# Performance work log

Hardware: AMD Instinct MI355X
Metric: run time of the kernel (lower is better)

The kernel has to match this reference:

```python
import jax, jax.numpy as jnp
import numpy as np

EMBED_DIM = 512
NUM_HEADS = 8
HEAD_DIM = EMBED_DIM // NUM_HEADS
SEQ = 1024
BSZ = 8
T1 = 0.6
T2 = 0.4
MAX_NEG = -jnp.finfo(jnp.float32).max


def setup_inputs() -> dict:
    key = jax.random.key(0)
    ks = jax.random.split(key, 10)
    shp = (SEQ, BSZ, EMBED_DIM)
    inv = 1.0 / np.sqrt(EMBED_DIM)
    return {
        "query": jax.random.normal(ks[0], shp, jnp.float32),
        "key": jax.random.normal(ks[1], shp, jnp.float32),
        "value": jax.random.normal(ks[2], shp, jnp.float32),
        "query_sem": jax.random.normal(ks[3], shp, jnp.float32),
        "key_sem": jax.random.normal(ks[4], shp, jnp.float32),
        "sem_map": jax.random.uniform(ks[5], (SEQ, SEQ), jnp.float32),
        "in_proj_weight": jax.random.normal(ks[6], (3 * EMBED_DIM, EMBED_DIM), jnp.float32) * inv,
        "in_proj_bias": jnp.zeros((3 * EMBED_DIM,), jnp.float32),
        "out_proj_weight": jax.random.normal(ks[7], (EMBED_DIM, EMBED_DIM), jnp.float32) * inv,
        "out_proj_bias": jnp.zeros((EMBED_DIM,), jnp.float32),
    }


def _heads(x):
    # [T, B, E] -> [B*H, T, head_dim]
    T, B, E = x.shape
    return jnp.transpose(x.reshape(T, B * NUM_HEADS, HEAD_DIM), (1, 0, 2))


def _attn_path(qx, kx, vx, sem_map, Wi, bi, Wo, bo, ssa):
    # packed in-projection (generic path: q, k, v are distinct tensors)
    Wq, Wk, Wv = jnp.split(Wi, 3, axis=0)
    bq, bk, bv = jnp.split(bi, 3)
    q = _heads(qx @ Wq.T + bq)
    k = _heads(kx @ Wk.T + bk)
    v = _heads(vx @ Wv.T + bv)
    scale = 1.0 / np.sqrt(HEAD_DIM)
    scores = jnp.einsum("bte,bse->bts", q * scale, k)  # [B*H, T, S]
    scores = jnp.where(sem_map[None, :, :] < 0.5, MAX_NEG, scores)
    if ssa:
        # keep only the argmax entry per row, others set to max_neg
        idx = jnp.argmax(scores, axis=-1)  # [B*H, T]
        keep = jnp.arange(scores.shape[-1])[None, None, :] == idx[..., None]
        scores = jnp.where(keep, scores, MAX_NEG)
    w = jax.nn.softmax(scores, axis=-1)
    o = jnp.einsum("bts,bse->bte", w, v)  # [B*H, T, head_dim]
    o = jnp.transpose(o, (1, 0, 2)).reshape(SEQ, BSZ, EMBED_DIM)
    return o @ Wo.T + bo


def reference(query, key, value, query_sem, key_sem, sem_map, in_proj_weight, in_proj_bias, out_proj_weight, out_proj_bias):
    # SCA: semantic q/k attend, style value
    x_sca = _attn_path(query_sem, key_sem, value, sem_map, in_proj_weight, in_proj_bias, out_proj_weight, out_proj_bias, ssa=False)
    # SSA: content/style q/k, hard-argmax sparsified attention
    x_ssa = _attn_path(query, key, value, sem_map, in_proj_weight, in_proj_bias, out_proj_weight, out_proj_bias, ssa=True)
    return T1 * x_sca + T2 * x_ssa
```

## Files before the change

### kernel.cpp

```cpp
#include <hip/hip_runtime.h>
#include <float.h>


namespace {
constexpr int kSeq = 1024;
constexpr int kBsz = 8;
constexpr int kEmb = 512;
constexpr int kHD  = 64;
constexpr float kT1 = 0.6f;
constexpr float kT2 = 0.4f;
constexpr float kScale = 0.125f;
constexpr float kMargin = 0.125f;
constexpr int kCap = 256;
}

typedef short bf16x8 __attribute__((ext_vector_type(8)));
typedef float f32x4  __attribute__((ext_vector_type(4)));

union FragU { uint4 u4; bf16x8 f; uint u[4]; };

__device__ __forceinline__ ushort f2bf(float f) {
  uint u = __float_as_uint(f);
  u += 0x7fff + ((u >> 16) & 1);
  return (ushort)(u >> 16);
}
__device__ __forceinline__ uint pack2(float lo, float hi) {
  return (uint)f2bf(lo) | ((uint)f2bf(hi) << 16);
}
__device__ __forceinline__ float bf2f(uint h) {
  return __uint_as_float(h << 16);
}
__device__ __forceinline__ uint monokey(float v) {
  uint u = __float_as_uint(v);
  return (u & 0x80000000u) ? ~u : (u | 0x80000000u);
}

__global__ void smask_prep(const float* __restrict__ SEM,
                           unsigned long long* __restrict__ SMASK) {
  const int t = blockIdx.x;
  const int w4 = threadIdx.x >> 6;
  const int lane = threadIdx.x & 63;
#pragma unroll
  for (int i = 0; i < 4; ++i) {
    const int word = (w4 << 2) + i;
    const float v = SEM[t * kSeq + (word << 6) + lane];
    unsigned long long m = __ballot(v >= 0.5f);
    if (lane == 0) SMASK[t * 16 + word] = m;
  }
}

__global__ __launch_bounds__(256, 4) void proj_v4(
    const float* __restrict__ Xq, const float* __restrict__ Xk,
    const float* __restrict__ W, const float* __restrict__ bias,
    float* __restrict__ OutQ, float* __restrict__ OutK,
    ushort* __restrict__ ShQ, ushort* __restrict__ ShK)
{
  __shared__ float As[32 * 132];
  __shared__ float Bs[32 * 68];

  const int z = blockIdx.z;
  const float* X = z ? Xk : Xq;
  float* Out = z ? OutK : OutQ;
  ushort* shadow = z ? ShK : ShQ;
  const int woff = z << 9;
  const float sscale = z ? 1.0f : kScale;

  const int mBase = blockIdx.x << 7;
  const int nBase = blockIdx.y << 6;
  const int tid = threadIdx.x;
  const int tx = tid & 15;
  const int my = tid >> 4;
  const int ar = tid >> 1, ah = (tid & 1) << 4;
  const int br = tid >> 2, bk = (tid & 3) << 3;

  float acc[8][4];
#pragma unroll
  for (int i = 0; i < 8; ++i)
#pragma unroll
    for (int j = 0; j < 4; ++j) acc[i][j] = 0.f;

  const float* xp = X + (size_t)(mBase + ar) * kEmb + ah;
  const float* wp = W + (size_t)(woff + nBase + br) * kEmb + bk;

  float4 a0 = ((const float4*)xp)[0];
  float4 a1 = ((const float4*)xp)[1];
  float4 a2 = ((const float4*)xp)[2];
  float4 a3 = ((const float4*)xp)[3];
  float4 b0 = ((const float4*)wp)[0];
  float4 b1 = ((const float4*)wp)[1];

  for (int k0 = 0; k0 < kEmb; k0 += 32) {
    __syncthreads();
    {
      float av[16] = {a0.x, a0.y, a0.z, a0.w, a1.x, a1.y, a1.z, a1.w,
                      a2.x, a2.y, a2.z, a2.w, a3.x, a3.y, a3.z, a3.w};
#pragma unroll
      for (int i = 0; i < 16; ++i) As[(ah + i) * 132 + ar] = av[i];
      float bv[8] = {b0.x, b0.y, b0.z, b0.w, b1.x, b1.y, b1.z, b1.w};
#pragma unroll
      for (int i = 0; i < 8; ++i) Bs[(bk + i) * 68 + br] = bv[i];
    }
    __syncthreads();

    const int kn = k0 + 32;
    if (kn < kEmb) {
      a0 = ((const float4*)(xp + kn))[0];
      a1 = ((const float4*)(xp + kn))[1];
      a2 = ((const float4*)(xp + kn))[2];
      a3 = ((const float4*)(xp + kn))[3];
      b0 = ((const float4*)(wp + kn))[0];
      b1 = ((const float4*)(wp + kn))[1];
    }

#pragma unroll 8
    for (int k = 0; k < 32; ++k) {
      float4 A0 = *(const float4*)&As[k * 132 + (my << 3)];
      float4 A1 = *(const float4*)&As[k * 132 + (my << 3) + 4];
      float4 Bv = *(const float4*)&Bs[k * 68 + (tx << 2)];
      float aa[8] = {A0.x, A0.y, A0.z, A0.w, A1.x, A1.y, A1.z, A1.w};
      float bb[4] = {Bv.x, Bv.y, Bv.z, Bv.w};
#pragma unroll
      for (int i = 0; i < 8; ++i)
#pragma unroll
        for (int j = 0; j < 4; ++j)
          acc[i][j] = fmaf(aa[i], bb[j], acc[i][j]);
    }
  }

#pragma unroll
  for (int i = 0; i < 8; ++i) {
    const int m = mBase + (my << 3) + i;
#pragma unroll
    for (int j = 0; j < 4; ++j) {
      const int n = nBase + (tx << 2) + j;
      const float v = acc[i][j] + bias[woff + n];
      const int oi = (((m & 7) << 3) + (n >> 6)) * (kSeq * kHD) +
                     ((m >> 3) << 6) + (n & 63);
      Out[oi] = v;
      shadow[oi] = f2bf(v * sscale);
    }
  }
}

__global__ __launch_bounds__(256, 4) void gemm_bf16(
    const float* __restrict__ X0, const float* __restrict__ X1,
    const float* __restrict__ X2, const ushort* __restrict__ X16,
    const float* __restrict__ W, const float* __restrict__ bias,
    float* __restrict__ OutF, ushort* __restrict__ Out16,
    int woffBase, int aMode, int outMode, float scale0)
{
  __shared__ uint As[128 * 20];
  __shared__ uint Bs[64 * 20];

  const int z = blockIdx.z;
  const float* X = (z == 0) ? X0 : (z == 1) ? X1 : X2;
  const int woff = woffBase + (z << 9);
  const float scale = (z == 0) ? scale0 : 1.0f;
  const size_t zoff = (size_t)z * ((size_t)kSeq * kBsz * kEmb);

  const int mBase = blockIdx.x << 7;
  const int nBase = blockIdx.y << 6;
  const int tid = threadIdx.x;
  const int w = tid >> 6;
  const int l = tid & 63;
  const int l15 = l & 15;
  const int quad = l >> 4;
  const int wm = w & 1, wn = w >> 1;

  const int srow = tid >> 1;
  const int shalf = tid & 1;

  f32x4 acc[4][2];
#pragma unroll
  for (int mi = 0; mi < 4; ++mi)
#pragma unroll
    for (int ni = 0; ni < 2; ++ni) acc[mi][ni] = (f32x4){0.f, 0.f, 0.f, 0.f};

  uint4 qa0, qa1;
  float4 ra0, ra1, ra2, ra3;
  float4 rb0, rb1, rb2, rb3;

#define GLOAD(kk) do {                                                     \
    if (aMode == 2) {                                                      \
      const uint* src_ = (const uint*)X16 + (size_t)(mBase + srow) * 256 + \
                         ((kk) >> 1) + (shalf << 3);                       \
      qa0 = ((const uint4*)src_)[0];                                       \
      qa1 = ((const uint4*)src_)[1];                                       \
    } else {                                                               \
      const float* xp_ = X + (size_t)(mBase + srow) * kEmb + (kk) +        \
                         (shalf << 4);                                     \
      ra0 = ((const float4*)xp_)[0];                                       \
      ra1 = ((const float4*)xp_)[1];                                       \
      ra2 = ((const float4*)xp_)[2];                                       \
      ra3 = ((const float4*)xp_)[3];                                       \
    }                                                                      \
    if (tid < 128) {                                                       \
      const float* wp_ = W + (size_t)(woff + nBase + srow) * kEmb + (kk) + \
                         (shalf << 4);                                     \
      rb0 = ((const float4*)wp_)[0];                                       \
      rb1 = ((const float4*)wp_)[1];                                       \
      rb2 = ((const float4*)wp_)[2];                                       \
      rb3 = ((const float4*)wp_)[3];                                       \
    }                                                                      \
  } while (0)

  GLOAD(0);

  for (int k0 = 0; k0 < kEmb; k0 += 32) {
    uint4 ah0, ah1, bw0, bw1;
    if (aMode == 2) {
      ah0 = qa0; ah1 = qa1;
    } else {
      ah0 = make_uint4(pack2(ra0.x, ra0.y), pack2(ra0.z, ra0.w),
                       pack2(ra1.x, ra1.y), pack2(ra1.z, ra1.w));
      ah1 = make_uint4(pack2(ra2.x, ra2.y), pack2(ra2.z, ra2.w),
                       pack2(ra3.x, ra3.y), pack2(ra3.z, ra3.w));
    }
    if (tid < 128) {
      bw0 = make_uint4(pack2(rb0.x, rb0.y), pack2(rb0.z, rb0.w),
                       pack2(rb1.x, rb1.y), pack2(rb1.z, rb1.w));
      bw1 = make_uint4(pack2(rb2.x, rb2.y), pack2(rb2.z, rb2.w),
                       pack2(rb3.x, rb3.y), pack2(rb3.z, rb3.w));
    }
    __syncthreads();
    {
      uint* dst = As + srow * 20 + (shalf << 3);
      ((uint4*)dst)[0] = ah0;
      ((uint4*)dst)[1] = ah1;
      if (tid < 128) {
        uint* db = Bs + srow * 20 + (shalf << 3);
        ((uint4*)db)[0] = bw0;
        ((uint4*)db)[1] = bw1;
      }
    }
    __syncthreads();

    if (k0 + 32 < kEmb) GLOAD(k0 + 32);

    FragU aF[4], bF[2];
#pragma unroll
    for (int ni = 0; ni < 2; ++ni)
      bF[ni].u4 = *(const uint4*)(Bs + ((wn << 5) + (ni << 4) + l15) * 20 + (quad << 2));
#pragma unroll
    for (int mi = 0; mi < 4; ++mi)
      aF[mi].u4 = *(const uint4*)(As + ((wm << 6) + (mi << 4) + l15) * 20 + (quad << 2));
#pragma unroll
    for (int mi = 0; mi < 4; ++mi)
#pragma unroll
      for (int ni = 0; ni < 2; ++ni)
        acc[mi][ni] = __builtin_amdgcn_mfma_f32_16x16x32_bf16(
            aF[mi].f, bF[ni].f, acc[mi][ni], 0, 0, 0);
  }
#undef GLOAD

#pragma unroll
  for (int ni = 0; ni < 2; ++ni) {
    const int n = nBase + (wn << 5) + (ni << 4) + l15;
    const float bv = bias[woff + n];
#pragma unroll
    for (int mi = 0; mi < 4; ++mi) {
#pragma unroll
      for (int r = 0; r < 4; ++r) {
        const int m = mBase + (wm << 6) + (mi << 4) + (quad << 2) + r;
        const float v = acc[mi][ni][r] + bv;
        if (outMode == 0) {
          OutF[(size_t)m * kEmb + n] = v;
        } else {
          const int oi = (((m & 7) << 3) + (n >> 6)) * (kSeq * kHD) +
                         ((m >> 3) << 6) + (n & 63);
          Out16[zoff + oi] = f2bf(v * scale);
        }
      }
    }
  }
}

__global__ __launch_bounds__(256, 4) void sca_mfma2(
    const ushort* __restrict__ Q16, const ushort* __restrict__ K16,
    const ushort* __restrict__ V16,
    const unsigned long long* __restrict__ SMASK,
    ushort* __restrict__ MIX16)
{
  __shared__ uint ks[64 * 36];
  __shared__ uint vt[64 * 36];
  __shared__ uint ps[4][16 * 36];

  const int t0  = blockIdx.x << 6;
  const int bh  = blockIdx.y;
  const int tid = threadIdx.x;
  const int w    = tid >> 6;
  const int l    = tid & 63;
  const int l15  = l & 15;
  const int quad = l >> 4;

  const uint* Qu = (const uint*)Q16 + (size_t)bh * (kSeq * 32);
  const uint* Ku = (const uint*)K16 + (size_t)bh * (kSeq * 32);
  const uint* Vu = (const uint*)V16 + (size_t)bh * (kSeq * 32);

  FragU qf0, qf1;
  {
    const uint* qrow = Qu + (size_t)(t0 + (w << 4) + l15) * 32;
    qf0.u4 = *(const uint4*)(qrow + (quad << 2));
    qf1.u4 = *(const uint4*)(qrow + 16 + (quad << 2));
  }

  f32x4 oacc[4];
#pragma unroll
  for (int nt = 0; nt < 4; ++nt) oacc[nt] = (f32x4){0.f, 0.f, 0.f, 0.f};
  float den[4] = {0.f, 0.f, 0.f, 0.f};

  uint* psw = ps[w];

  const int sl = tid >> 2, c = tid & 3;
  const int p = tid >> 3, c7 = tid & 7;

  uint4 pk0 = ((const uint4*)(Ku + (size_t)sl * 32 + (c << 3)))[0];
  uint4 pk1 = ((const uint4*)(Ku + (size_t)sl * 32 + (c << 3)))[1];
  uint4 pv0 = *(const uint4*)(Vu + (size_t)(p << 1) * 32 + (c7 << 2));
  uint4 pv1 = *(const uint4*)(Vu + (size_t)(p << 1) * 32 + (c7 << 2) + 32);

  for (int s0 = 0, tile = 0; s0 < kSeq; s0 += 64, ++tile) {
    __syncthreads();
    {
      uint* dst = ks + sl * 36 + (c << 3);
      ((uint4*)dst)[0] = pk0;
      ((uint4*)dst)[1] = pk1;
    }
    {
      FragU A, B;
      A.u4 = pv0;
      B.u4 = pv1;
      const int Wp = (p + ((c7 & 3) << 2)) & 31;
#pragma unroll
      for (int i = 0; i < 8; ++i) {
        uint ai = (A.u[i >> 1] >> ((i & 1) << 4)) & 0xFFFF;
        uint bi = (B.u[i >> 1] >> ((i & 1) << 4)) & 0xFFFF;
        vt[((c7 << 3) + i) * 36 + Wp] = ai | (bi << 16);
      }
    }
    __syncthreads();

    if (s0 + 64 < kSeq) {
      const uint* kp = Ku + (size_t)(s0 + 64 + sl) * 32 + (c << 3);
      pk0 = ((const uint4*)kp)[0];
      pk1 = ((const uint4*)kp)[1];
      const uint* va = Vu + (size_t)(s0 + 64 + (p << 1)) * 32 + (c7 << 2);
      pv0 = *(const uint4*)va;
      pv1 = *(const uint4*)(va + 32);
    }

    unsigned long long wv[4];
#pragma unroll
    for (int r = 0; r < 4; ++r)
      wv[r] = SMASK[(size_t)(t0 + (w << 4) + (quad << 2) + r) * 16 + tile];

#pragma unroll
    for (int st = 0; st < 4; ++st) {
      f32x4 sacc = (f32x4){0.f, 0.f, 0.f, 0.f};
      const int srow = (st << 4) + l15;
      FragU kf0, kf1;
      kf0.u4 = *(const uint4*)(ks + srow * 36 + (quad << 2));
      kf1.u4 = *(const uint4*)(ks + srow * 36 + 16 + (quad << 2));
      sacc = __builtin_amdgcn_mfma_f32_16x16x32_bf16(qf0.f, kf0.f, sacc, 0, 0, 0);
      sacc = __builtin_amdgcn_mfma_f32_16x16x32_bf16(qf1.f, kf1.f, sacc, 0, 0, 0);

#pragma unroll
      for (int r = 0; r < 4; ++r) {
        const int trow = (quad << 2) + r;
        const uint bit = (uint)(wv[r] >> ((st << 4) + l15)) & 1u;
        const float val = bit ? __expf(sacc[r]) : 0.f;
        den[r] += val;
        const int W  = (st << 3) + (l15 >> 1);
        const int Wp = (W + (((trow >> 3) & 1) << 3)) & 31;
        ushort* p16 = (ushort*)(psw + trow * 36 + Wp);
        p16[l15 & 1] = f2bf(val);
      }
    }
#pragma unroll
    for (int ch = 0; ch < 2; ++ch) {
      FragU pf;
      const int pw = ((ch << 4) + (quad << 2) + (((l15 >> 3) & 1) << 3)) & 31;
      pf.u4 = *(const uint4*)(psw + l15 * 36 + pw);
#pragma unroll
      for (int nt = 0; nt < 4; ++nt) {
        const int d = (nt << 4) + l15;
        const int vw = ((ch << 4) + (quad << 2) + (((d >> 3) & 3) << 2)) & 31;
        FragU vf;
        vf.u4 = *(const uint4*)(vt + d * 36 + vw);
        oacc[nt] = __builtin_amdgcn_mfma_f32_16x16x32_bf16(pf.f, vf.f, oacc[nt], 0, 0, 0);
      }
    }
  }

#pragma unroll
  for (int r = 0; r < 4; ++r) {
    float d = den[r];
    d += __shfl_xor(d, 1);
    d += __shfl_xor(d, 2);
    d += __shfl_xor(d, 4);
    d += __shfl_xor(d, 8);
    den[r] = kT1 / d;
  }
  const int b = bh >> 3, h = bh & 7;
#pragma unroll
  for (int nt = 0; nt < 4; ++nt) {
#pragma unroll
    for (int r = 0; r < 4; ++r) {
      const int t = t0 + (w << 4) + (quad << 2) + r;
      const int d = (nt << 4) + l15;
      MIX16[(size_t)(t * kBsz + b) * kEmb + (h << 6) + d] =
          f2bf(oacc[nt][r] * den[r]);
    }
  }
}

__global__ __launch_bounds__(512, 4) void ssa_v3(
    const ushort* __restrict__ Q16, const ushort* __restrict__ K16,
    const float* __restrict__ Qf, const float* __restrict__ Kf,
    const ushort* __restrict__ V16,
    const unsigned long long* __restrict__ SMASK,
    ushort* __restrict__ MIX16)
{
  __shared__ uint ks[64 * 36];
  __shared__ uint2 list[8][kCap];
  __shared__ float thrL[8][16];
  __shared__ unsigned long long key64L[8][16];
  __shared__ uint cnt[8];

  const int t0  = blockIdx.x << 7;
  const int bh  = blockIdx.y;
  const int tid = threadIdx.x;
  const int w    = tid >> 6;
  const int l    = tid & 63;
  const int l15  = l & 15;
  const int quad = l >> 4;

  if (tid < 8) cnt[tid] = 0;
  if (tid < 128) ((unsigned long long*)key64L)[tid] = 0ull;

  const uint* Qu = (const uint*)Q16 + (size_t)bh * (kSeq * 32);
  const uint* Ku = (const uint*)K16 + (size_t)bh * (kSeq * 32);

  FragU qf0, qf1;
  {
    const uint* qrow = Qu + (size_t)(t0 + (w << 4) + l15) * 32;
    qf0.u4 = *(const uint4*)(qrow + (quad << 2));
    qf1.u4 = *(const uint4*)(qrow + 16 + (quad << 2));
  }

  float m4[4] = {-FLT_MAX, -FLT_MAX, -FLT_MAX, -FLT_MAX};

  const int krow = tid >> 3, kc = tid & 7;
  uint4 pk = *(const uint4*)(Ku + (size_t)krow * 32 + (kc << 2));

  for (int s0 = 0, tile = 0; s0 < kSeq; s0 += 64, ++tile) {
    __syncthreads();
    *(uint4*)(ks + krow * 36 + (kc << 2)) = pk;
    __syncthreads();

    if (s0 + 64 < kSeq)
      pk = *(const uint4*)(Ku + (size_t)(s0 + 64 + krow) * 32 + (kc << 2));

    unsigned long long wv[4];
#pragma unroll
    for (int r = 0; r < 4; ++r)
      wv[r] = SMASK[(size_t)(t0 + (w << 4) + (quad << 2) + r) * 16 + tile];

    f32x4 sv[4];
#pragma unroll
    for (int st = 0; st < 4; ++st) {
      f32x4 sacc = (f32x4){0.f, 0.f, 0.f, 0.f};
      const int srow = (st << 4) + l15;
      FragU kf0, kf1;
      kf0.u4 = *(const uint4*)(ks + srow * 36 + (quad << 2));
      kf1.u4 = *(const uint4*)(ks + srow * 36 + 16 + (quad << 2));
      sacc = __builtin_amdgcn_mfma_f32_16x16x32_bf16(qf0.f, kf0.f, sacc, 0, 0, 0);
      sacc = __builtin_amdgcn_mfma_f32_16x16x32_bf16(qf1.f, kf1.f, sacc, 0, 0, 0);
      sv[st] = sacc;
#pragma unroll
      for (int r = 0; r < 4; ++r) {
        const uint bit = (uint)(wv[r] >> ((st << 4) + l15)) & 1u;
        if (bit) m4[r] = fmaxf(m4[r], sacc[r]);
      }
    }
#pragma unroll
    for (int r = 0; r < 4; ++r) {
      float m = m4[r];
      m = fmaxf(m, __shfl_xor(m, 1));
      m = fmaxf(m, __shfl_xor(m, 2));
      m = fmaxf(m, __shfl_xor(m, 4));
      m = fmaxf(m, __shfl_xor(m, 8));
      m4[r] = m;
    }
#pragma unroll
    for (int st = 0; st < 4; ++st) {
#pragma unroll
      for (int r = 0; r < 4; ++r) {
        const uint bit = (uint)(wv[r] >> ((st << 4) + l15)) & 1u;
        const float x = sv[st][r];
        if (bit && x >= m4[r] - kMargin) {
          uint idx = atomicAdd(&cnt[w], 1u);
          if (idx < (uint)kCap) {
            const int rowid = (quad << 2) + r;
            const int s = s0 + (st << 4) + l15;
            list[w][idx] = make_uint2(__float_as_uint(x),
                                      ((uint)rowid << 10) | (uint)s);
          }
        }
      }
    }
  }

  if (l15 == 0) {
#pragma unroll
    for (int r = 0; r < 4; ++r) thrL[w][(quad << 2) + r] = m4[r] - kMargin;
  }
  __syncthreads();

  const uint n = min(cnt[w], (uint)kCap);
  const float* Qbf = Qf + (size_t)bh * (kSeq * kHD);
  const float* Kbf = Kf + (size_t)bh * (kSeq * kHD);
  for (uint base = 0; base < n; base += 64) {
    const uint e = base + (uint)l;
    if (e < n) {
      const uint2 ent = list[w][e];
      const uint rowid = ent.y >> 10;
      const uint s = ent.y & 1023u;
      const float xv = __uint_as_float(ent.x);
      if (xv >= thrL[w][rowid]) {
        const int t = t0 + (w << 4) + (int)rowid;
        const float* qe = Qbf + (size_t)t * kHD;
        const float* ke = Kbf + (size_t)s * kHD;
        float p0 = 0.f, p1 = 0.f, p2 = 0.f, p3 = 0.f;
#pragma unroll
        for (int i = 0; i < 16; ++i) {
          float4 qq = *(const float4*)(qe + (i << 2));
          float4 kk = *(const float4*)(ke + (i << 2));
          p0 = fmaf(qq.x, kk.x, p0);
          p1 = fmaf(qq.y, kk.y, p1);
          p2 = fmaf(qq.z, kk.z, p2);
          p3 = fmaf(qq.w, kk.w, p3);
        }
        const float acc = ((p0 + p1) + (p2 + p3)) * kScale;
        const unsigned long long key =
            ((unsigned long long)monokey(acc) << 16) |
            (unsigned long long)(1023u - s);
        atomicMax(&key64L[w][rowid], key);
      }
    }
  }
  __syncthreads();

  const int b = bh >> 3, h = bh & 7;
  const uint* Vu = (const uint*)V16 + (size_t)bh * (kSeq * 32);
#pragma unroll
  for (int r = 0; r < 4; ++r) {
    const int rowid = (quad << 2) + r;
    const unsigned long long key = key64L[w][rowid];
    const uint s = 1023u - (uint)(key & 0xFFFFull);
    const uint2 vv = *(const uint2*)(Vu + (size_t)s * 32 + (l15 << 1));
    const int t = t0 + (w << 4) + rowid;
    uint* op = (uint*)MIX16 + ((size_t)(t * kBsz + b) * kEmb + (h << 6)) / 2 + (l15 << 1);
    uint2 o = *(uint2*)op;
    float o0 = bf2f(o.x & 0xFFFF) + kT2 * bf2f(vv.x & 0xFFFF);
    float o1 = bf2f(o.x >> 16)    + kT2 * bf2f(vv.x >> 16);
    float o2 = bf2f(o.y & 0xFFFF) + kT2 * bf2f(vv.y & 0xFFFF);
    float o3 = bf2f(o.y >> 16)    + kT2 * bf2f(vv.y >> 16);
    *(uint2*)op = make_uint2(pack2(o0, o1), pack2(o2, o3));
  }
}

extern "C" void kernel_launch(void* const* d_in, const int* in_sizes, int n_in,
                              void* d_out, int out_size, void* d_ws, size_t ws_size,
                              hipStream_t stream) {
  const float* query  = (const float*)d_in[0];
  const float* key    = (const float*)d_in[1];
  const float* value  = (const float*)d_in[2];
  const float* qsem   = (const float*)d_in[3];
  const float* ksem   = (const float*)d_in[4];
  const float* semmap = (const float*)d_in[5];
  const float* Wi     = (const float*)d_in[6];
  const float* bi     = (const float*)d_in[7];
  const float* Wo     = (const float*)d_in[8];
  const float* bo     = (const float*)d_in[9];
  float* out = (float*)d_out;

  char* ws = (char*)d_ws;
  unsigned long long* SMASK = (unsigned long long*)ws;          ws += 1024 * 16 * 8;
  ushort* Q16  = (ushort*)ws;  ws += (size_t)64 * kSeq * kHD * 2;
  ushort* K16  = (ushort*)ws;  ws += (size_t)64 * kSeq * kHD * 2;
  ushort* V16  = (ushort*)ws;  ws += (size_t)64 * kSeq * kHD * 2;
  ushort* MIX16 = (ushort*)ws; ws += (size_t)kSeq * kBsz * kEmb * 2;
  float* P1 = (float*)ws;      ws += (size_t)64 * kSeq * kHD * 4;
  float* P0 = out;

  const dim3 gp(64, 8, 2);
  const dim3 g3(64, 8, 3);
  const dim3 gb(64, 8);
  const dim3 gs(16, 64);
  const dim3 gv(8, 64);

  smask_prep<<<1024, 256, 0, stream>>>(semmap, SMASK);
  gemm_bf16<<<g3, 256, 0, stream>>>(qsem, ksem, value, nullptr, Wi, bi,
                                    nullptr, Q16, 0, 0, 1, kScale);
  sca_mfma2<<<gs, 256, 0, stream>>>(Q16, K16, V16, SMASK, MIX16);
  proj_v4<<<gp, 256, 0, stream>>>(query, key, Wi, bi, P0, P1, Q16, K16);
  ssa_v3<<<gv, 512, 0, stream>>>(Q16, K16, P0, P1, V16, SMASK, MIX16);
  gemm_bf16<<<gb, 256, 0, stream>>>(nullptr, nullptr, nullptr, MIX16, Wo, bo,
                                    out, nullptr, 0, 2, 0, 1.0f);
}
```

Baseline: 407.1 us.

## Fuse projection kernels and run SCA/SSA attention concurrently in shared launches

Merges the fp32 SSA projection and the bf16 SCA projection into one launch by assigning block roles, and puts SCA attention and SSA argmax blocks in a single launch so they run concurrently. The SSA path now builds its bf16 Q/K fragments from the fp32 projections instead of shadow bf16 copies. SSA writes its selected V rows to a separate buffer, and the output GEMM combines MIX and SSA values on load, which removes the read-modify-write dependency between the two attention kernels. The aim is to cut launch count and serialization and let heterogeneous blocks fill the GPU. The cost is an extra bf16 buffer, extra conversion work in SSA, and SSA blocks now covering half as many rows with 256 threads.

```diff
diff --git a/kernel.cpp b/kernel.cpp
--- a/kernel.cpp
+++ b/kernel.cpp
@@ -34,6 +34,11 @@
   uint u = __float_as_uint(v);
   return (u & 0x80000000u) ? ~u : (u | 0x80000000u);
 }
+__device__ __forceinline__ uint combine2(uint m, uint s) {
+  float lo = bf2f(m & 0xFFFF) + kT2 * bf2f(s & 0xFFFF);
+  float hi = bf2f(m >> 16)    + kT2 * bf2f(s >> 16);
+  return pack2(lo, hi);
+}
 
 __global__ void smask_prep(const float* __restrict__ SEM,
                            unsigned long long* __restrict__ SMASK) {
@@ -49,24 +54,18 @@
   }
 }
 
-__global__ __launch_bounds__(256, 4) void proj_v4(
+__device__ __forceinline__ void proj_body(
+    float* As, float* Bs, int bx, int by, int z,
     const float* __restrict__ Xq, const float* __restrict__ Xk,
     const float* __restrict__ W, const float* __restrict__ bias,
-    float* __restrict__ OutQ, float* __restrict__ OutK,
-    ushort* __restrict__ ShQ, ushort* __restrict__ ShK)
+    float* __restrict__ OutQ, float* __restrict__ OutK)
 {
-  __shared__ float As[32 * 132];
-  __shared__ float Bs[32 * 68];
-
-  const int z = blockIdx.z;
   const float* X = z ? Xk : Xq;
   float* Out = z ? OutK : OutQ;
-  ushort* shadow = z ? ShK : ShQ;
   const int woff = z << 9;
-  const float sscale = z ? 1.0f : kScale;
-
-  const int mBase = blockIdx.x << 7;
-  const int nBase = blockIdx.y << 6;
+
+  const int mBase = bx << 7;
+  const int nBase = by << 6;
   const int tid = threadIdx.x;
   const int tx = tid & 15;
   const int my = tid >> 4;
@@ -137,29 +136,24 @@
       const int oi = (((m & 7) << 3) + (n >> 6)) * (kSeq * kHD) +
                      ((m >> 3) << 6) + (n & 63);
       Out[oi] = v;
-      shadow[oi] = f2bf(v * sscale);
-    }
-  }
-}
-
-__global__ __launch_bounds__(256, 4) void gemm_bf16(
+    }
+  }
+}
+
+__device__ __forceinline__ void gemm_sca_body(
+    uint* As, uint* Bs, int bx, int by, int z,
     const float* __restrict__ X0, const float* __restrict__ X1,
-    const float* __restrict__ X2, const ushort* __restrict__ X16,
+    const float* __restrict__ X2,
     const float* __restrict__ W, const float* __restrict__ bias,
-    float* __restrict__ OutF, ushort* __restrict__ Out16,
-    int woffBase, int aMode, int outMode, float scale0)
+    ushort* __restrict__ Out16)
 {
-  __shared__ uint As[128 * 20];
-  __shared__ uint Bs[64 * 20];
-
-  const int z = blockIdx.z;
   const float* X = (z == 0) ? X0 : (z == 1) ? X1 : X2;
-  const int woff = woffBase + (z << 9);
-  const float scale = (z == 0) ? scale0 : 1.0f;
+  const int woff = z << 9;
+  const float scale = (z == 0) ? kScale : 1.0f;
   const size_t zoff = (size_t)z * ((size_t)kSeq * kBsz * kEmb);
 
-  const int mBase = blockIdx.x << 7;
-  const int nBase = blockIdx.y << 6;
+  const int mBase = bx << 7;
+  const int nBase = by << 6;
   const int tid = threadIdx.x;
   const int w = tid >> 6;
   const int l = tid & 63;
@@ -176,24 +170,16 @@
 #pragma unroll
     for (int ni = 0; ni < 2; ++ni) acc[mi][ni] = (f32x4){0.f, 0.f, 0.f, 0.f};
 
-  uint4 qa0, qa1;
   float4 ra0, ra1, ra2, ra3;
   float4 rb0, rb1, rb2, rb3;
 
-#define GLOAD(kk) do {                                                     \
-    if (aMode == 2) {                                                      \
-      const uint* src_ = (const uint*)X16 + (size_t)(mBase + srow) * 256 + \
-                         ((kk) >> 1) + (shalf << 3);                       \
-      qa0 = ((const uint4*)src_)[0];                                       \
-      qa1 = ((const uint4*)src_)[1];                                       \
-    } else {                                                               \
-      const float* xp_ = X + (size_t)(mBase + srow) * kEmb + (kk) +        \
-                         (shalf << 4);                                     \
-      ra0 = ((const float4*)xp_)[0];                                       \
-      ra1 = ((const float4*)xp_)[1];                                       \
-      ra2 = ((const float4*)xp_)[2];                                       \
-      ra3 = ((const float4*)xp_)[3];                                       \
-    }                                                                      \
+#define GLOADF(kk) do {                                                    \
+    const float* xp_ = X + (size_t)(mBase + srow) * kEmb + (kk) +          \
+                       (shalf << 4);                                       \
+    ra0 = ((const float4*)xp_)[0];                                         \
+    ra1 = ((const float4*)xp_)[1];                                         \
+    ra2 = ((const float4*)xp_)[2];                                         \
+    ra3 = ((const float4*)xp_)[3];                                         \
     if (tid < 128) {                                                       \
       const float* wp_ = W + (size_t)(woff + nBase + srow) * kEmb + (kk) + \
                          (shalf << 4);                                     \
@@ -204,18 +190,14 @@
     }                                                                      \
   } while (0)
 
-  GLOAD(0);
+  GLOADF(0);
 
   for (int k0 = 0; k0 < kEmb; k0 += 32) {
     uint4 ah0, ah1, bw0, bw1;
-    if (aMode == 2) {
-      ah0 = qa0; ah1 = qa1;
-    } else {
-      ah0 = make_uint4(pack2(ra0.x, ra0.y), pack2(ra0.z, ra0.w),
-                       pack2(ra1.x, ra1.y), pack2(ra1.z, ra1.w));
-      ah1 = make_uint4(pack2(ra2.x, ra2.y), pack2(ra2.z, ra2.w),
-                       pack2(ra3.x, ra3.y), pack2(ra3.z, ra3.w));
-    }
+    ah0 = make_uint4(pack2(ra0.x, ra0.y), pack2(ra0.z, ra0.w),
+                     pack2(ra1.x, ra1.y), pack2(ra1.z, ra1.w));
+    ah1 = make_uint4(pack2(ra2.x, ra2.y), pack2(ra2.z, ra2.w),
+                     pack2(ra3.x, ra3.y), pack2(ra3.z, ra3.w));
     if (tid < 128) {
       bw0 = make_uint4(pack2(rb0.x, rb0.y), pack2(rb0.z, rb0.w),
                        pack2(rb1.x, rb1.y), pack2(rb1.z, rb1.w));
@@ -235,7 +217,7 @@
     }
     __syncthreads();
 
-    if (k0 + 32 < kEmb) GLOAD(k0 + 32);
+    if (k0 + 32 < kEmb) GLOADF(k0 + 32);
 
     FragU aF[4], bF[2];
 #pragma unroll
@@ -251,7 +233,7 @@
         acc[mi][ni] = __builtin_amdgcn_mfma_f32_16x16x32_bf16(
             aF[mi].f, bF[ni].f, acc[mi][ni], 0, 0, 0);
   }
-#undef GLOAD
+#undef GLOADF
 
 #pragma unroll
   for (int ni = 0; ni < 2; ++ni) {
@@ -263,30 +245,43 @@
       for (int r = 0; r < 4; ++r) {
         const int m = mBase + (wm << 6) + (mi << 4) + (quad << 2) + r;
         const float v = acc[mi][ni][r] + bv;
-        if (outMode == 0) {
-          OutF[(size_t)m * kEmb + n] = v;
-        } else {
-          const int oi = (((m & 7) << 3) + (n >> 6)) * (kSeq * kHD) +
-                         ((m >> 3) << 6) + (n & 63);
-          Out16[zoff + oi] = f2bf(v * scale);
-        }
-      }
-    }
-  }
-}
-
-__global__ __launch_bounds__(256, 4) void sca_mfma2(
+        const int oi = (((m & 7) << 3) + (n >> 6)) * (kSeq * kHD) +
+                       ((m >> 3) << 6) + (n & 63);
+        Out16[zoff + oi] = f2bf(v * scale);
+      }
+    }
+  }
+}
+
+__global__ __launch_bounds__(256, 4) void front_fused(
+    const float* __restrict__ query, const float* __restrict__ key,
+    const float* __restrict__ qsem, const float* __restrict__ ksem,
+    const float* __restrict__ value,
+    const float* __restrict__ Wi, const float* __restrict__ bi,
+    float* __restrict__ P0, float* __restrict__ P1,
+    ushort* __restrict__ Q16)
+{
+  __shared__ float smem[6400];
+
+  const int bid = blockIdx.x;
+  const int g = bid / 5, s = bid % 5;
+  const int bx = g & 63, by = g >> 6;
+  if (s < 2) {
+    proj_body(smem, smem + 4224, bx, by, s, query, key, Wi, bi, P0, P1);
+  } else {
+    gemm_sca_body((uint*)smem, (uint*)smem + 2560, bx, by, s - 2,
+                  qsem, ksem, value, Wi, bi, Q16);
+  }
+}
+
+__device__ __forceinline__ void sca_body(
+    uint* ks, uint* vt, uint* ps, int idx, int bh,
     const ushort* __restrict__ Q16, const ushort* __restrict__ K16,
     const ushort* __restrict__ V16,
     const unsigned long long* __restrict__ SMASK,
     ushort* __restrict__ MIX16)
 {
-  __shared__ uint ks[64 * 36];
-  __shared__ uint vt[64 * 36];
-  __shared__ uint ps[4][16 * 36];
-
-  const int t0  = blockIdx.x << 6;
-  const int bh  = blockIdx.y;
+  const int t0  = idx << 6;
   const int tid = threadIdx.x;
   const int w    = tid >> 6;
   const int l    = tid & 63;
@@ -309,7 +304,7 @@
   for (int nt = 0; nt < 4; ++nt) oacc[nt] = (f32x4){0.f, 0.f, 0.f, 0.f};
   float den[4] = {0.f, 0.f, 0.f, 0.f};
 
-  uint* psw = ps[w];
+  uint* psw = ps + w * 576;
 
   const int sl = tid >> 2, c = tid & 3;
   const int p = tid >> 3, c7 = tid & 7;
@@ -414,52 +409,73 @@
   }
 }
 
-__global__ __launch_bounds__(512, 4) void ssa_v3(
-    const ushort* __restrict__ Q16, const ushort* __restrict__ K16,
+__device__ __forceinline__ void ssa_body(
+    uint* ks, uint2* list2, float* thrL, unsigned long long* key64,
+    uint* cnt, int idx, int bh,
     const float* __restrict__ Qf, const float* __restrict__ Kf,
     const ushort* __restrict__ V16,
     const unsigned long long* __restrict__ SMASK,
-    ushort* __restrict__ MIX16)
+    ushort* __restrict__ SSAV16)
 {
-  __shared__ uint ks[64 * 36];
-  __shared__ uint2 list[8][kCap];
-  __shared__ float thrL[8][16];
-  __shared__ unsigned long long key64L[8][16];
-  __shared__ uint cnt[8];
-
-  const int t0  = blockIdx.x << 7;
-  const int bh  = blockIdx.y;
+  const int t0  = idx << 6;
   const int tid = threadIdx.x;
   const int w    = tid >> 6;
   const int l    = tid & 63;
   const int l15  = l & 15;
   const int quad = l >> 4;
 
-  if (tid < 8) cnt[tid] = 0;
-  if (tid < 128) ((unsigned long long*)key64L)[tid] = 0ull;
-
-  const uint* Qu = (const uint*)Q16 + (size_t)bh * (kSeq * 32);
-  const uint* Ku = (const uint*)K16 + (size_t)bh * (kSeq * 32);
+  if (tid < 4) cnt[tid] = 0;
+  if (tid < 64) key64[tid] = 0ull;
+
+  const float* Qh = Qf + (size_t)bh * (kSeq * kHD);
+  const float* Kh = Kf + (size_t)bh * (kSeq * kHD);
 
   FragU qf0, qf1;
   {
-    const uint* qrow = Qu + (size_t)(t0 + (w << 4) + l15) * 32;
-    qf0.u4 = *(const uint4*)(qrow + (quad << 2));
-    qf1.u4 = *(const uint4*)(qrow + 16 + (quad << 2));
+    const float* qrow = Qh + (size_t)(t0 + (w << 4) + l15) * kHD;
+    float4 q0 = *(const float4*)(qrow + (quad << 3));
+    float4 q1 = *(const float4*)(qrow + (quad << 3) + 4);
+    float4 q2 = *(const float4*)(qrow + 32 + (quad << 3));
+    float4 q3 = *(const float4*)(qrow + 32 + (quad << 3) + 4);
+    qf0.u4 = make_uint4(pack2(q0.x * kScale, q0.y * kScale),
+                        pack2(q0.z * kScale, q0.w * kScale),
+                        pack2(q1.x * kScale, q1.y * kScale),
+                        pack2(q1.z * kScale, q1.w * kScale));
+    qf1.u4 = make_uint4(pack2(q2.x * kScale, q2.y * kScale),
+                        pack2(q2.z * kScale, q2.w * kScale),
+                        pack2(q3.x * kScale, q3.y * kScale),
+                        pack2(q3.z * kScale, q3.w * kScale));
   }
 
   float m4[4] = {-FLT_MAX, -FLT_MAX, -FLT_MAX, -FLT_MAX};
 
-  const int krow = tid >> 3, kc = tid & 7;
-  uint4 pk = *(const uint4*)(Ku + (size_t)krow * 32 + (kc << 2));
+  const int sl = tid >> 2, c4 = tid & 3;
+  const float* kp = Kh + (size_t)sl * kHD + (c4 << 4);
+  float4 pk0 = ((const float4*)kp)[0];
+  float4 pk1 = ((const float4*)kp)[1];
+  float4 pk2 = ((const float4*)kp)[2];
+  float4 pk3 = ((const float4*)kp)[3];
 
   for (int s0 = 0, tile = 0; s0 < kSeq; s0 += 64, ++tile) {
     __syncthreads();
-    *(uint4*)(ks + krow * 36 + (kc << 2)) = pk;
-    __syncthreads();
-
-    if (s0 + 64 < kSeq)
-      pk = *(const uint4*)(Ku + (size_t)(s0 + 64 + krow) * 32 + (kc << 2));
+    {
+      uint4 w0 = make_uint4(pack2(pk0.x, pk0.y), pack2(pk0.z, pk0.w),
+                            pack2(pk1.x, pk1.y), pack2(pk1.z, pk1.w));
+      uint4 w1 = make_uint4(pack2(pk2.x, pk2.y), pack2(pk2.z, pk2.w),
+                            pack2(pk3.x, pk3.y), pack2(pk3.z, pk3.w));
+      uint* dst = ks + sl * 36 + (c4 << 3);
+      ((uint4*)dst)[0] = w0;
+      ((uint4*)dst)[1] = w1;
+    }
+    __syncthreads();
+
+    if (s0 + 64 < kSeq) {
+      const float* kn = Kh + (size_t)(s0 + 64 + sl) * kHD + (c4 << 4);
+      pk0 = ((const float4*)kn)[0];
+      pk1 = ((const float4*)kn)[1];
+      pk2 = ((const float4*)kn)[2];
+      pk3 = ((const float4*)kn)[3];
+    }
 
     unsigned long long wv[4];
 #pragma unroll
@@ -499,12 +515,12 @@
         const uint bit = (uint)(wv[r] >> ((st << 4) + l15)) & 1u;
         const float x = sv[st][r];
         if (bit && x >= m4[r] - kMargin) {
-          uint idx = atomicAdd(&cnt[w], 1u);
-          if (idx < (uint)kCap) {
+          uint idx2 = atomicAdd(&cnt[w], 1u);
+          if (idx2 < (uint)kCap) {
             const int rowid = (quad << 2) + r;
             const int s = s0 + (st << 4) + l15;
-            list[w][idx] = make_uint2(__float_as_uint(x),
-                                      ((uint)rowid << 10) | (uint)s);
+            list2[w * kCap + idx2] = make_uint2(__float_as_uint(x),
+                                                ((uint)rowid << 10) | (uint)s);
           }
         }
       }
@@ -513,24 +529,22 @@
 
   if (l15 == 0) {
 #pragma unroll
-    for (int r = 0; r < 4; ++r) thrL[w][(quad << 2) + r] = m4[r] - kMargin;
+    for (int r = 0; r < 4; ++r) thrL[w * 16 + (quad << 2) + r] = m4[r] - kMargin;
   }
   __syncthreads();
 
   const uint n = min(cnt[w], (uint)kCap);
-  const float* Qbf = Qf + (size_t)bh * (kSeq * kHD);
-  const float* Kbf = Kf + (size_t)bh * (kSeq * kHD);
   for (uint base = 0; base < n; base += 64) {
     const uint e = base + (uint)l;
     if (e < n) {
-      const uint2 ent = list[w][e];
+      const uint2 ent = list2[w * kCap + e];
       const uint rowid = ent.y >> 10;
       const uint s = ent.y & 1023u;
       const float xv = __uint_as_float(ent.x);
-      if (xv >= thrL[w][rowid]) {
+      if (xv >= thrL[w * 16 + rowid]) {
         const int t = t0 + (w << 4) + (int)rowid;
-        const float* qe = Qbf + (size_t)t * kHD;
-        const float* ke = Kbf + (size_t)s * kHD;
+        const float* qe = Qh + (size_t)t * kHD;
+        const float* ke = Kh + (size_t)s * kHD;
         float p0 = 0.f, p1 = 0.f, p2 = 0.f, p3 = 0.f;
 #pragma unroll
         for (int i = 0; i < 16; ++i) {
@@ -545,7 +559,7 @@
         const unsigned long long key =
             ((unsigned long long)monokey(acc) << 16) |
             (unsigned long long)(1023u - s);
-        atomicMax(&key64L[w][rowid], key);
+        atomicMax(&key64[w * 16 + rowid], key);
       }
     }
   }
@@ -556,17 +570,145 @@
 #pragma unroll
   for (int r = 0; r < 4; ++r) {
     const int rowid = (quad << 2) + r;
-    const unsigned long long key = key64L[w][rowid];
+    const unsigned long long key = key64[w * 16 + rowid];
     const uint s = 1023u - (uint)(key & 0xFFFFull);
     const uint2 vv = *(const uint2*)(Vu + (size_t)s * 32 + (l15 << 1));
     const int t = t0 + (w << 4) + rowid;
-    uint* op = (uint*)MIX16 + ((size_t)(t * kBsz + b) * kEmb + (h << 6)) / 2 + (l15 << 1);
-    uint2 o = *(uint2*)op;
-    float o0 = bf2f(o.x & 0xFFFF) + kT2 * bf2f(vv.x & 0xFFFF);
-    float o1 = bf2f(o.x >> 16)    + kT2 * bf2f(vv.x >> 16);
-    float o2 = bf2f(o.y & 0xFFFF) + kT2 * bf2f(vv.y & 0xFFFF);
-    float o3 = bf2f(o.y >> 16)    + kT2 * bf2f(vv.y >> 16);
-    *(uint2*)op = make_uint2(pack2(o0, o1), pack2(o2, o3));
+    uint* op = (uint*)SSAV16 + ((size_t)(t * kBsz + b) * kEmb + (h << 6)) / 2 + (l15 << 1);
+    *(uint2*)op = vv;
+  }
+}
+
+__global__ __launch_bounds__(256, 4) void back_fused(
+    const ushort* __restrict__ Q16, const ushort* __restrict__ K16,
+    const ushort* __restrict__ V16,
+    const float* __restrict__ P0, const float* __restrict__ P1,
+    const unsigned long long* __restrict__ SMASK,
+    ushort* __restrict__ MIX16, ushort* __restrict__ SSAV16)
+{
+  __shared__ unsigned long long lds8[3456];
+  uint* base = (uint*)lds8;
+
+  const int role = blockIdx.x & 1;
+  const int idx  = blockIdx.x >> 1;
+  const int bh   = blockIdx.y;
+
+  if (role == 0) {
+    sca_body(base, base + 2304, base + 4608, idx, bh,
+             Q16, K16, V16, SMASK, MIX16);
+  } else {
+    ssa_body(base, (uint2*)(base + 2304), (float*)(base + 4352),
+             (unsigned long long*)(base + 4416), base + 4544,
+             idx, bh, P0, P1, V16, SMASK, SSAV16);
+  }
+}
+
+__global__ __launch_bounds__(256, 4) void gemm_out(
+    const ushort* __restrict__ MIX16, const ushort* __restrict__ SSAV16,
+    const float* __restrict__ W, const float* __restrict__ bias,
+    float* __restrict__ OutF)
+{
+  __shared__ uint As[128 * 20];
+  __shared__ uint Bs[64 * 20];
+
+  const int mBase = blockIdx.x << 7;
+  const int nBase = blockIdx.y << 6;
+  const int tid = threadIdx.x;
+  const int w = tid >> 6;
+  const int l = tid & 63;
+  const int l15 = l & 15;
+  const int quad = l >> 4;
+  const int wm = w & 1, wn = w >> 1;
+
+  const int srow = tid >> 1;
+  const int shalf = tid & 1;
+
+  f32x4 acc[4][2];
+#pragma unroll
+  for (int mi = 0; mi < 4; ++mi)
+#pragma unroll
+    for (int ni = 0; ni < 2; ++ni) acc[mi][ni] = (f32x4){0.f, 0.f, 0.f, 0.f};
+
+  uint4 qa0, qa1, qb0, qb1;
+  float4 rb0, rb1, rb2, rb3;
+
+#define GLOADO(kk) do {                                                    \
+    const size_t off_ = (size_t)(mBase + srow) * 256 + ((kk) >> 1) +       \
+                        (shalf << 3);                                      \
+    const uint* ma_ = (const uint*)MIX16 + off_;                           \
+    qa0 = ((const uint4*)ma_)[0];                                          \
+    qa1 = ((const uint4*)ma_)[1];                                          \
+    const uint* sa_ = (const uint*)SSAV16 + off_;                          \
+    qb0 = ((const uint4*)sa_)[0];                                          \
+    qb1 = ((const uint4*)sa_)[1];                                          \
+    if (tid < 128) {                                                       \
+      const float* wp_ = W + (size_t)(nBase + srow) * kEmb + (kk) +        \
+                         (shalf << 4);                                     \
+      rb0 = ((const float4*)wp_)[0];                                       \
+      rb1 = ((const float4*)wp_)[1];                                       \
+      rb2 = ((const float4*)wp_)[2];                                       \
+      rb3 = ((const float4*)wp_)[3];                                       \
+    }                                                                      \
+  } while (0)
+
+  GLOADO(0);
+
+  for (int k0 = 0; k0 < kEmb; k0 += 32) {
+    uint4 ah0, ah1, bw0, bw1;
+    ah0 = make_uint4(combine2(qa0.x, qb0.x), combine2(qa0.y, qb0.y),
+                     combine2(qa0.z, qb0.z), combine2(qa0.w, qb0.w));
+    ah1 = make_uint4(combine2(qa1.x, qb1.x), combine2(qa1.y, qb1.y),
+                     combine2(qa1.z, qb1.z), combine2(qa1.w, qb1.w));
+    if (tid < 128) {
+      bw0 = make_uint4(pack2(rb0.x, rb0.y), pack2(rb0.z, rb0.w),
+                       pack2(rb1.x, rb1.y), pack2(rb1.z, rb1.w));
+      bw1 = make_uint4(pack2(rb2.x, rb2.y), pack2(rb2.z, rb2.w),
+                       pack2(rb3.x, rb3.y), pack2(rb3.z, rb3.w));
+    }
+    __syncthreads();
+    {
+      uint* dst = As + srow * 20 + (shalf << 3);
+      ((uint4*)dst)[0] = ah0;
+      ((uint4*)dst)[1] = ah1;
+      if (tid < 128) {
+        uint* db = Bs + srow * 20 + (shalf << 3);
+        ((uint4*)db)[0] = bw0;
+        ((uint4*)db)[1] = bw1;
+      }
+    }
+    __syncthreads();
+
+    if (k0 + 32 < kEmb) GLOADO(k0 + 32);
+
+    FragU aF[4], bF[2];
+#pragma unroll
+    for (int ni = 0; ni < 2; ++ni)
+      bF[ni].u4 = *(const uint4*)(Bs + ((wn << 5) + (ni << 4) + l15) * 20 + (quad << 2));
+#pragma unroll
+    for (int mi = 0; mi < 4; ++mi)
+      aF[mi].u4 = *(const uint4*)(As + ((wm << 6) + (mi << 4) + l15) * 20 + (quad << 2));
+#pragma unroll
+    for (int mi = 0; mi < 4; ++mi)
+#pragma unroll
+      for (int ni = 0; ni < 2; ++ni)
+        acc[mi][ni] = __builtin_amdgcn_mfma_f32_16x16x32_bf16(
+            aF[mi].f, bF[ni].f, acc[mi][ni], 0, 0, 0);
+  }
+#undef GLOADO
+
+#pragma unroll
+  for (int ni = 0; ni < 2; ++ni) {
+    const int n = nBase + (wn << 5) + (ni << 4) + l15;
+    const float bv = bias[n];
+#pragma unroll
+    for (int mi = 0; mi < 4; ++mi) {
+#pragma unroll
+      for (int r = 0; r < 4; ++r) {
+        const int m = mBase + (wm << 6) + (mi << 4) + (quad << 2) + r;
+        const float v = acc[mi][ni][r] + bv;
+        OutF[(size_t)m * kEmb + n] = v;
+      }
+    }
   }
 }
 
@@ -586,26 +728,19 @@
   float* out = (float*)d_out;
 
   char* ws = (char*)d_ws;
-  unsigned long long* SMASK = (unsigned long long*)ws;          ws += 1024 * 16 * 8;
-  ushort* Q16  = (ushort*)ws;  ws += (size_t)64 * kSeq * kHD * 2;
-  ushort* K16  = (ushort*)ws;  ws += (size_t)64 * kSeq * kHD * 2;
-  ushort* V16  = (ushort*)ws;  ws += (size_t)64 * kSeq * kHD * 2;
+  unsigned long long* SMASK = (unsigned long long*)ws;           ws += 1024 * 16 * 8;
+  ushort* Q16   = (ushort*)ws; ws += (size_t)64 * kSeq * kHD * 2;
+  ushort* K16   = (ushort*)ws; ws += (size_t)64 * kSeq * kHD * 2;
+  ushort* V16   = (ushort*)ws; ws += (size_t)64 * kSeq * kHD * 2;
   ushort* MIX16 = (ushort*)ws; ws += (size_t)kSeq * kBsz * kEmb * 2;
+  ushort* SSAV16= (ushort*)ws; ws += (size_t)kSeq * kBsz * kEmb * 2;
   float* P1 = (float*)ws;      ws += (size_t)64 * kSeq * kHD * 4;
   float* P0 = out;
 
-  const dim3 gp(64, 8, 2);
-  const dim3 g3(64, 8, 3);
-  const dim3 gb(64, 8);
-  const dim3 gs(16, 64);
-  const dim3 gv(8, 64);
-
   smask_prep<<<1024, 256, 0, stream>>>(semmap, SMASK);
-  gemm_bf16<<<g3, 256, 0, stream>>>(qsem, ksem, value, nullptr, Wi, bi,
-                                    nullptr, Q16, 0, 0, 1, kScale);
-  sca_mfma2<<<gs, 256, 0, stream>>>(Q16, K16, V16, SMASK, MIX16);
-  proj_v4<<<gp, 256, 0, stream>>>(query, key, Wi, bi, P0, P1, Q16, K16);
-  ssa_v3<<<gv, 512, 0, stream>>>(Q16, K16, P0, P1, V16, SMASK, MIX16);
-  gemm_bf16<<<gb, 256, 0, stream>>>(nullptr, nullptr, nullptr, MIX16, Wo, bo,
-                                    out, nullptr, 0, 2, 0, 1.0f);
-}
+  front_fused<<<2560, 256, 0, stream>>>(query, key, qsem, ksem, value,
+                                        Wi, bi, P0, P1, Q16);
+  back_fused<<<dim3(32, 64), 256, 0, stream>>>(Q16, K16, V16, P0, P1,
+                                               SMASK, MIX16, SSAV16);
+  gemm_out<<<dim3(64, 8), 256, 0, stream>>>(MIX16, SSAV16, Wo, bo, out);
+}
```

Result: no change. 413.4 us (+1.5%).
